# Kernel optimization log

Hardware: AMD Instinct MI355X
Metric: run time of the kernel (lower is better)

Reference implementation:

```python
import jax, jax.numpy as jnp
import numpy as np

B, N, CIN, C = 2, 400000, 192, 128
Y, X, Z = 512, 512, 40
EPS1 = 1e-5   # default BatchNorm1d eps for feature_proj
EPS2 = 1e-3   # norm_fn eps=0.001 for shared_conv BN


def setup_inputs() -> dict:
    key = jax.random.key(0)
    ks = jax.random.split(key, 12)
    voxel_features = jax.random.normal(ks[0], (N, CIN), jnp.float32)
    bi = jax.random.randint(ks[1], (N,), 0, B)
    zi = jax.random.randint(ks[2], (N,), 0, Z)
    yi = jax.random.randint(ks[3], (N,), 0, Y)
    xi = jax.random.randint(ks[4], (N,), 0, X)
    voxel_coords = jnp.stack([bi, zi, yi, xi], axis=1).astype(jnp.int32)  # (N,4)=[b,z,y,x]
    # feature_proj: Linear(CIN->C) + BN1d (inference stats) + ReLU
    W_proj = jax.random.normal(ks[5], (CIN, C), jnp.float32) * np.float32(1.0 / np.sqrt(CIN))
    b_proj = jnp.zeros((C,), jnp.float32)
    bn1_gamma = jnp.ones((C,), jnp.float32)
    bn1_beta = jnp.zeros((C,), jnp.float32)
    bn1_mean = jax.random.normal(ks[6], (C,), jnp.float32) * np.float32(0.1)
    bn1_var = jax.random.uniform(ks[7], (C,), jnp.float32, 0.5, 1.5)
    # shared_conv: SubMConv2d(C,C,3,pad=1,bias) + BN(eps=1e-3) + ReLU
    conv_w = jax.random.normal(ks[8], (3, 3, C, C), jnp.float32) * np.float32(1.0 / np.sqrt(9 * C))
    conv_b = jnp.zeros((C,), jnp.float32)
    bn2_gamma = jnp.ones((C,), jnp.float32)
    bn2_beta = jnp.zeros((C,), jnp.float32)
    bn2_mean = jax.random.normal(ks[9], (C,), jnp.float32) * np.float32(0.1)
    bn2_var = jax.random.uniform(ks[10], (C,), jnp.float32, 0.5, 1.5)
    return dict(voxel_features=voxel_features, voxel_coords=voxel_coords,
                W_proj=W_proj, b_proj=b_proj,
                bn1_gamma=bn1_gamma, bn1_beta=bn1_beta, bn1_mean=bn1_mean, bn1_var=bn1_var,
                conv_w=conv_w, conv_b=conv_b,
                bn2_gamma=bn2_gamma, bn2_beta=bn2_beta, bn2_mean=bn2_mean, bn2_var=bn2_var)


def reference(voxel_features, voxel_coords, W_proj, b_proj,
              bn1_gamma, bn1_beta, bn1_mean, bn1_var,
              conv_w, conv_b, bn2_gamma, bn2_beta, bn2_mean, bn2_var):
    # 1) feature_proj (Linear + BN1d inference + ReLU)
    f = voxel_features @ W_proj + b_proj                      # (N, C)
    f = (f - bn1_mean) * jax.lax.rsqrt(bn1_var + EPS1) * bn1_gamma + bn1_beta
    f = jax.nn.relu(f)
    # 2) bev_aggregate: unique([b,y,x]) + index_add == scatter-sum to dense BEV grid
    bi, yi, xi = voxel_coords[:, 0], voxel_coords[:, 2], voxel_coords[:, 3]
    dense = jnp.zeros((B, Y, X, C), f.dtype).at[bi, yi, xi].add(f)
    active = jnp.zeros((B, Y, X), bool).at[bi, yi, xi].set(True)
    # 3) SubMConv2d(3x3, pad=1) + BN + ReLU; subm == dense conv masked to active sites
    out = jax.lax.conv_general_dilated(dense, conv_w, (1, 1), 'SAME',
                                       dimension_numbers=('NHWC', 'HWIO', 'NHWC')) + conv_b
    out = (out - bn2_mean) * jax.lax.rsqrt(bn2_var + EPS2) * bn2_gamma + bn2_beta
    out = jax.nn.relu(out)
    # sparse tensor only holds active sites; zero elsewhere
    return jnp.where(active[..., None], out, jnp.float32(0.0))  # (B, Y, X, C)
```

## Files before the change

### kernel.cpp

```cpp
#include <hip/hip_runtime.h>

#define Bq 2
#define Yq 512
#define Xq 512
#define NVOX 400000

typedef __bf16 bf16x8 __attribute__((ext_vector_type(8)));
typedef float f32x4 __attribute__((ext_vector_type(4)));
typedef float f32x16 __attribute__((ext_vector_type(16)));
typedef short s16x8 __attribute__((ext_vector_type(8)));
typedef short s16x2 __attribute__((ext_vector_type(2)));

__device__ __forceinline__ short f2bf_s(float f){
    return __builtin_bit_cast(short, static_cast<__bf16>(f));
}

__device__ __forceinline__ void atomic_pk_add_bf16(short* addr, unsigned data){
#if __has_builtin(__builtin_amdgcn_global_atomic_fadd_v2bf16)
    s16x2 v; v[0] = (short)(data & 0xffff); v[1] = (short)(data >> 16);
    __builtin_amdgcn_global_atomic_fadd_v2bf16(
        (__attribute__((address_space(1))) s16x2*)addr, v);
#else
    asm volatile("global_atomic_pk_add_bf16 %0, %1, off"
                 :: "v"(addr), "v"(data) : "memory");
#endif
}

__global__ void kprep(const float* __restrict__ conv_w, const float* __restrict__ W_proj,
                      short* __restrict__ wTs, short* __restrict__ wpT){
    int tid = blockIdx.x*256 + threadIdx.x;
    if (tid < 9*128*128){
        int tap = tid >> 14; int r = tid & 16383; int co = r >> 7; int ci = r & 127;
        int g = ci >> 3, e = ci & 7;
        wTs[tap*16384 + co*128 + (((g & 8) | ((g & 7) ^ (co & 7))) << 3) + e] =
            f2bf_s(conv_w[tap*16384 + ci*128 + co]);
    }
    int e = tid - 9*128*128;
    if (e >= 0 && e < 128*192){
        int co = e / 192; int ci = e - co*192;
        wpT[e] = f2bf_s(W_proj[ci*128 + co]);
    }
}

__global__ void kcount(const int* __restrict__ vc, unsigned* __restrict__ cnt,
                       unsigned char* __restrict__ act){
    int i = blockIdx.x*256 + threadIdx.x;
    if (i >= NVOX) return;
    const int4 c = *reinterpret_cast<const int4*>(vc + i*4);
    int cell = (c.x*Yq + c.z)*Xq + c.w;
    act[cell] = 1;
    atomicAdd(&cnt[cell], 1u);
}

__global__ void __launch_bounds__(256, 2)
kproj(const float* __restrict__ vf, const int* __restrict__ vc,
      const unsigned* __restrict__ cnt,
      const short* __restrict__ wpT, const float* __restrict__ bp,
      const float* __restrict__ g1, const float* __restrict__ be1,
      const float* __restrict__ mu1, const float* __restrict__ va1,
      short* __restrict__ dbf){
    __shared__ char smem[64*200*2];
    __shared__ int cellsPk[64];
    short*    A  = (short*)smem;
    unsigned* st = (unsigned*)smem;
    const int t = threadIdx.x;
    const int v0 = blockIdx.x * 64;

    const float4* vf4 = reinterpret_cast<const float4*>(vf);
    #pragma unroll
    for (int j = 0; j < 12; ++j){
        int i = t + j*256;
        int v = i / 48, kq = i - v*48;
        float4 x = vf4[(size_t)(v0 + v)*48 + kq];
        short4 s; s.x=f2bf_s(x.x); s.y=f2bf_s(x.y); s.z=f2bf_s(x.z); s.w=f2bf_s(x.w);
        *reinterpret_cast<short4*>(&A[v*200 + kq*4]) = s;
    }
    if (t < 64){
        int vi = v0 + t;
        int bi = vc[vi*4 + 0], yi = vc[vi*4 + 2], xi = vc[vi*4 + 3];
        unsigned cn = cnt[(bi*Yq + yi)*Xq + xi];
        int P = (bi*514 + (yi + 1))*514 + (xi + 1);
        cellsPk[t] = (P*8 + ((xi + 1) & 7)) | ((cn > 1) ? (1 << 30) : 0);
    }
    __syncthreads();

    const int w  = t >> 6;
    const int l  = t & 63;
    const int lr = l & 15;
    const int q  = l >> 4;

    const short* wp_lane = wpT + (size_t)(w*32 + lr)*192 + q*8;
    bf16x8 bb[2][6];
    #pragma unroll
    for (int n = 0; n < 2; ++n)
        #pragma unroll
        for (int kc = 0; kc < 6; ++kc)
            bb[n][kc] = *reinterpret_cast<const bf16x8*>(wp_lane + n*16*192 + kc*32);

    f32x4 acc[4][2] = {};
    #pragma unroll
    for (int kc = 0; kc < 6; ++kc){
        bf16x8 a[4];
        #pragma unroll
        for (int m = 0; m < 4; ++m)
            a[m] = *reinterpret_cast<const bf16x8*>(&A[(m*16 + lr)*200 + kc*32 + q*8]);
        #pragma unroll
        for (int m = 0; m < 4; ++m)
            #pragma unroll
            for (int n = 0; n < 2; ++n)
                acc[m][n] = __builtin_amdgcn_mfma_f32_16x16x32_bf16(a[m], bb[n][kc], acc[m][n], 0, 0, 0);
    }

    __syncthreads();
    const int odd = lr & 1;
    #pragma unroll
    for (int n = 0; n < 2; ++n){
        int c = w*32 + n*16 + lr;
        float s1  = g1[c] * rsqrtf(va1[c] + 1e-5f);
        float sh1 = be1[c] + (bp[c] - mu1[c]) * s1;
        int jj = w*16 + n*8 + (lr >> 1);
        #pragma unroll
        for (int m = 0; m < 4; ++m){
            #pragma unroll
            for (int r = 0; r < 4; ++r){
                int vx = m*16 + q*4 + r;
                float val = fmaxf(fmaf(acc[m][n][r], s1, sh1), 0.f);
                float vp  = __shfl_xor(val, 1);
                if (!odd){
                    unsigned data = (unsigned)(unsigned short)f2bf_s(val)
                                  | ((unsigned)(unsigned short)f2bf_s(vp) << 16);
                    st[vx*68 + jj] = data;
                }
            }
        }
    }
    __syncthreads();

    unsigned* dbf_u32 = reinterpret_cast<unsigned*>(dbf);
    #pragma unroll
    for (int i = 0; i < 16; ++i){
        int vv = w*16 + i;
        int pk = cellsPk[vv];
        int multi = pk >> 30;
        int P = (pk & 0x3fffffff) >> 3, xp7 = pk & 7;
        unsigned data = st[vv*68 + l];
        size_t idx = (size_t)P*64 + (((l >> 2) ^ xp7) << 2) + (l & 3);
        if (multi){
            if (data) atomic_pk_add_bf16((short*)(dbf_u32 + idx), data);
        } else {
            dbf_u32[idx] = data;
        }
    }
}

__global__ void __launch_bounds__(512, 2)
kconv(const short* __restrict__ dbf, const short* __restrict__ wTs,
      const unsigned char* __restrict__ act, const float* __restrict__ cb,
      const float* __restrict__ g2, const float* __restrict__ be2,
      const float* __restrict__ mu2, const float* __restrict__ va2,
      float* __restrict__ out){
    __shared__ short Atile[5*1056*8];
    __shared__ short Bbuf[4][1024*8];
    const int t = threadIdx.x;
    const int bid = (blockIdx.x & 7)*256 + (blockIdx.x >> 3);
    const int b   = bid >> 10;
    const int rem = bid & 1023;
    const int y0  = (rem >> 3) << 2;
    const int x0  = (rem & 7) << 6;

    const int w   = t >> 6, l = t & 63;
    const int yy  = w >> 1, nn = w & 1;
    const int l31 = l & 31, hi = l >> 5;
    const int wbase16 = w*64*16;

    #define STAGE_B(BUF, H) do {                                              \
        const short* gb = wTs + (size_t)((H) >> 1)*16384 + ((H) & 1)*64;      \
        _Pragma("unroll")                                                     \
        for (int j = 0; j < 2; ++j){                                          \
            int S = j*512 + t;                                                \
            const short* gp = gb + (S >> 3)*128 + (S & 7)*8;                  \
            __builtin_amdgcn_global_load_lds(                                 \
                (const __attribute__((address_space(1))) void*)gp,            \
                (__attribute__((address_space(3))) void*)                    \
                    ((char*)Bbuf[BUF] + (size_t)(j*512*16) + wbase16), 16, 0, 0); \
        }                                                                     \
    } while(0)

    STAGE_B(0, 0);
    STAGE_B(1, 1);
    #pragma unroll
    for (int j = 0; j < 11; ++j){
        int S = j*512 + t;
        if (S < 5280){
            int r = S / 1056, s = S - r*1056;
            const short* gp = dbf + ((size_t)((b*514 + (y0 + r))*514 + x0)*16 + s)*8;
            __builtin_amdgcn_global_load_lds(
                (const __attribute__((address_space(1))) void*)gp,
                (__attribute__((address_space(3))) void*)
                    ((char*)Atile + (size_t)(j*512*16) + wbase16), 16, 0, 0);
        }
    }

    f32x16 acc[2][2] = {};
    const int bReadBase = (nn*64 + l31)*64;
    const int bXor = l31 & 7;

    #pragma unroll
    for (int p = 0; p < 18; ++p){
        if ((p & 1) == 0){
            __builtin_amdgcn_sched_barrier(0);
            asm volatile("s_waitcnt vmcnt(0)" ::: "memory");
            __builtin_amdgcn_s_barrier();
            __builtin_amdgcn_sched_barrier(0);
            if (p + 2 < 18) STAGE_B((p+2) & 3, p+2);
            if (p + 3 < 18) STAGE_B((p+3) & 3, p+3);
            if (p == 6){
                #pragma unroll
                for (int j = 0; j < 3; ++j){
                    int S = j*512 + t;
                    if (S < 1056){
                        const short* gp = dbf + ((size_t)((b*514 + (y0 + 5))*514 + x0)*16 + S)*8;
                        __builtin_amdgcn_global_load_lds(
                            (const __attribute__((address_space(1))) void*)gp,
                            (__attribute__((address_space(3))) void*)
                                ((char*)Atile + (size_t)(j*512 + w*64)*16), 16, 0, 0);
                    }
                }
            }
            __builtin_amdgcn_sched_barrier(0);
        }
        const short* Bc = Bbuf[p & 3];
        const int tap = p >> 1, hh = p & 1;
        const int ky = tap / 3, kx = tap - ky*3;
        const int row = yy + ky;
        const int rowp = (row >= 5) ? 0 : row;
        const int p0 = l31 + kx, p1 = p0 + 32;
        const int base0 = (rowp*1056 + p0*16)*8;
        const int base1 = (rowp*1056 + p1*16)*8;
        const int pk7 = p0 & 7;
        #pragma unroll
        for (int kc = 0; kc < 4; ++kc){
            const int ks  = kc*2 + hi;
            const int q   = ((hh*8 + ks) ^ pk7) << 3;
            const int qb  = (ks ^ bXor) << 3;
            bf16x8 a0 = *reinterpret_cast<const bf16x8*>(&Atile[base0 + q]);
            bf16x8 a1 = *reinterpret_cast<const bf16x8*>(&Atile[base1 + q]);
            bf16x8 b0 = *reinterpret_cast<const bf16x8*>(&Bc[bReadBase + qb]);
            bf16x8 b1 = *reinterpret_cast<const bf16x8*>(&Bc[bReadBase + 2048 + qb]);
            acc[0][0] = __builtin_amdgcn_mfma_f32_32x32x16_bf16(a0, b0, acc[0][0], 0, 0, 0);
            acc[0][1] = __builtin_amdgcn_mfma_f32_32x32x16_bf16(a0, b1, acc[0][1], 0, 0, 0);
            acc[1][0] = __builtin_amdgcn_mfma_f32_32x32x16_bf16(a1, b0, acc[1][0], 0, 0, 0);
            acc[1][1] = __builtin_amdgcn_mfma_f32_32x32x16_bf16(a1, b1, acc[1][1], 0, 0, 0);
        }
    }
    #undef STAGE_B

    const int yg = y0 + yy;
    const size_t rowcell = (size_t)(b*Yq + yg)*Xq + x0;
    #pragma unroll
    for (int ni = 0; ni < 2; ++ni){
        int c = nn*64 + ni*32 + l31;
        float s2  = g2[c] * rsqrtf(va2[c] + 1e-3f);
        float sh2 = be2[c] + (cb[c] - mu2[c]) * s2;
        #pragma unroll
        for (int mi = 0; mi < 2; ++mi){
            #pragma unroll
            for (int r = 0; r < 16; ++r){
                int pos = mi*32 + (r & 3) + ((r >> 2) << 3) + hi*4;
                size_t cell = rowcell + pos;
                float v = act[cell] ? fmaxf(fmaf(acc[mi][ni][r], s2, sh2), 0.f) : 0.f;
                out[cell*128 + c] = v;
            }
        }
    }
}

extern "C" void kernel_launch(void* const* d_in, const int* in_sizes, int n_in,
                              void* d_out, int out_size, void* d_ws, size_t ws_size,
                              hipStream_t stream){
    const float* vf  = (const float*)d_in[0];
    const int*   vc  = (const int*)  d_in[1];
    const float* Wp  = (const float*)d_in[2];
    const float* bp  = (const float*)d_in[3];
    const float* g1  = (const float*)d_in[4];
    const float* be1 = (const float*)d_in[5];
    const float* mu1 = (const float*)d_in[6];
    const float* va1 = (const float*)d_in[7];
    const float* cw  = (const float*)d_in[8];
    const float* cb  = (const float*)d_in[9];
    const float* g2  = (const float*)d_in[10];
    const float* be2 = (const float*)d_in[11];
    const float* mu2 = (const float*)d_in[12];
    const float* va2 = (const float*)d_in[13];
    float* out = (float*)d_out;
    char* ws = (char*)d_ws;

    if (ws_size < 138233856ull) return;
    short* dbf = (short*)ws;
    unsigned char* act = (unsigned char*)(ws + 135268352);
    short* wTs = (short*)(ws + 135792640);
    short* wpT = (short*)(ws + 136087552);
    unsigned* cnt = (unsigned*)(ws + 136136704);

    hipMemsetAsync(dbf, 0, 135268352, stream);
    hipMemsetAsync(act, 0, 524288, stream);
    hipMemsetAsync(cnt, 0, 2097152, stream);
    kprep<<<672, 256, 0, stream>>>(cw, Wp, wTs, wpT);
    kcount<<<1563, 256, 0, stream>>>(vc, cnt, act);
    kproj<<<6250, 256, 0, stream>>>(vf, vc, cnt, wpT, bp, g1, be1, mu1, va1, dbf);
    kconv<<<2048, 512, 0, stream>>>(dbf, wTs, act, cb, g2, be2, mu2, va2, out);
}
```

Measured before the change: 358.5 us.

## Restructure subm conv: one row per block, weights held in registers per wave

Reworks the conv kernel so each 256-thread block computes one output row of 64 cells. Each wave owns 32 output channels and keeps its bf16 weight fragments in registers, double-buffered across taps and loaded directly from a reordered weight layout produced in the prep kernel. This removes LDS staging of weights and the per-tap barriers. In exchange, each block reloads three halo rows for a single output row, and every block re-reads the full weight set from cache, which raises input and weight traffic.

```diff
diff --git a/kernel.cpp b/kernel.cpp
--- a/kernel.cpp
+++ b/kernel.cpp
@@ -27,12 +27,13 @@
 }
 
 __global__ void kprep(const float* __restrict__ conv_w, const float* __restrict__ W_proj,
-                      short* __restrict__ wTs, short* __restrict__ wpT){
+                      short* __restrict__ wR, short* __restrict__ wpT){
     int tid = blockIdx.x*256 + threadIdx.x;
     if (tid < 9*128*128){
         int tap = tid >> 14; int r = tid & 16383; int co = r >> 7; int ci = r & 127;
-        int g = ci >> 3, e = ci & 7;
-        wTs[tap*16384 + co*128 + (((g & 8) | ((g & 7) ^ (co & 7))) << 3) + e] =
+        int nn = co >> 5, l31 = co & 31;
+        int kcc = ci >> 4, hi = (ci >> 3) & 1, j = ci & 7;
+        wR[(size_t)tap*16384 + nn*4096 + kcc*512 + (hi*32 + l31)*8 + j] =
             f2bf_s(conv_w[tap*16384 + ci*128 + co]);
     }
     int e = tid - 9*128*128;
@@ -153,124 +154,82 @@
     }
 }
 
-__global__ void __launch_bounds__(512, 2)
-kconv(const short* __restrict__ dbf, const short* __restrict__ wTs,
+__global__ void __launch_bounds__(256, 3)
+kconv(const short* __restrict__ dbf, const short* __restrict__ wR,
       const unsigned char* __restrict__ act, const float* __restrict__ cb,
       const float* __restrict__ g2, const float* __restrict__ be2,
       const float* __restrict__ mu2, const float* __restrict__ va2,
       float* __restrict__ out){
-    __shared__ short Atile[5*1056*8];
-    __shared__ short Bbuf[4][1024*8];
+    __shared__ short Atile[3*1056*8];
     const int t = threadIdx.x;
-    const int bid = (blockIdx.x & 7)*256 + (blockIdx.x >> 3);
-    const int b   = bid >> 10;
-    const int rem = bid & 1023;
-    const int y0  = (rem >> 3) << 2;
+    const int bid = (blockIdx.x & 7)*1024 + (blockIdx.x >> 3);
+    const int b   = bid >> 12;
+    const int rem = bid & 4095;
+    const int y   = rem >> 3;
     const int x0  = (rem & 7) << 6;
 
     const int w   = t >> 6, l = t & 63;
-    const int yy  = w >> 1, nn = w & 1;
     const int l31 = l & 31, hi = l >> 5;
-    const int wbase16 = w*64*16;
-
-    #define STAGE_B(BUF, H) do {                                              \
-        const short* gb = wTs + (size_t)((H) >> 1)*16384 + ((H) & 1)*64;      \
-        _Pragma("unroll")                                                     \
-        for (int j = 0; j < 2; ++j){                                          \
-            int S = j*512 + t;                                                \
-            const short* gp = gb + (S >> 3)*128 + (S & 7)*8;                  \
-            __builtin_amdgcn_global_load_lds(                                 \
-                (const __attribute__((address_space(1))) void*)gp,            \
-                (__attribute__((address_space(3))) void*)                    \
-                    ((char*)Bbuf[BUF] + (size_t)(j*512*16) + wbase16), 16, 0, 0); \
-        }                                                                     \
-    } while(0)
-
-    STAGE_B(0, 0);
-    STAGE_B(1, 1);
-    #pragma unroll
-    for (int j = 0; j < 11; ++j){
-        int S = j*512 + t;
-        if (S < 5280){
+
+    #pragma unroll
+    for (int j = 0; j < 13; ++j){
+        int S = j*256 + t;
+        if (S < 3168){
             int r = S / 1056, s = S - r*1056;
-            const short* gp = dbf + ((size_t)((b*514 + (y0 + r))*514 + x0)*16 + s)*8;
+            const short* gp = dbf + ((size_t)((b*514 + (y + r))*514 + x0)*16 + s)*8;
             __builtin_amdgcn_global_load_lds(
                 (const __attribute__((address_space(1))) void*)gp,
                 (__attribute__((address_space(3))) void*)
-                    ((char*)Atile + (size_t)(j*512*16) + wbase16), 16, 0, 0);
-        }
-    }
-
-    f32x16 acc[2][2] = {};
-    const int bReadBase = (nn*64 + l31)*64;
-    const int bXor = l31 & 7;
-
-    #pragma unroll
-    for (int p = 0; p < 18; ++p){
-        if ((p & 1) == 0){
-            __builtin_amdgcn_sched_barrier(0);
-            asm volatile("s_waitcnt vmcnt(0)" ::: "memory");
-            __builtin_amdgcn_s_barrier();
-            __builtin_amdgcn_sched_barrier(0);
-            if (p + 2 < 18) STAGE_B((p+2) & 3, p+2);
-            if (p + 3 < 18) STAGE_B((p+3) & 3, p+3);
-            if (p == 6){
-                #pragma unroll
-                for (int j = 0; j < 3; ++j){
-                    int S = j*512 + t;
-                    if (S < 1056){
-                        const short* gp = dbf + ((size_t)((b*514 + (y0 + 5))*514 + x0)*16 + S)*8;
-                        __builtin_amdgcn_global_load_lds(
-                            (const __attribute__((address_space(1))) void*)gp,
-                            (__attribute__((address_space(3))) void*)
-                                ((char*)Atile + (size_t)(j*512 + w*64)*16), 16, 0, 0);
-                    }
-                }
-            }
-            __builtin_amdgcn_sched_barrier(0);
-        }
-        const short* Bc = Bbuf[p & 3];
-        const int tap = p >> 1, hh = p & 1;
-        const int ky = tap / 3, kx = tap - ky*3;
-        const int row = yy + ky;
-        const int rowp = (row >= 5) ? 0 : row;
+                    ((char*)Atile + (size_t)(j*256 + w*64)*16), 16, 0, 0);
+        }
+    }
+
+    const short* wRb = wR + (size_t)w*4096 + l*8;
+    bf16x8 Breg[2][8];
+    #pragma unroll
+    for (int kcc = 0; kcc < 8; ++kcc)
+        Breg[0][kcc] = *reinterpret_cast<const bf16x8*>(wRb + kcc*512);
+
+    __syncthreads();
+
+    f32x16 acc[2] = {};
+
+    #pragma unroll
+    for (int tp = 0; tp < 9; ++tp){
+        if (tp < 8){
+            const short* wn = wRb + (size_t)(tp+1)*16384;
+            #pragma unroll
+            for (int kcc = 0; kcc < 8; ++kcc)
+                Breg[(tp+1) & 1][kcc] = *reinterpret_cast<const bf16x8*>(wn + kcc*512);
+        }
+        const int ky = tp / 3, kx = tp - ky*3;
         const int p0 = l31 + kx, p1 = p0 + 32;
-        const int base0 = (rowp*1056 + p0*16)*8;
-        const int base1 = (rowp*1056 + p1*16)*8;
+        const int base0 = (ky*1056 + p0*16)*8;
+        const int base1 = (ky*1056 + p1*16)*8;
         const int pk7 = p0 & 7;
         #pragma unroll
-        for (int kc = 0; kc < 4; ++kc){
-            const int ks  = kc*2 + hi;
-            const int q   = ((hh*8 + ks) ^ pk7) << 3;
-            const int qb  = (ks ^ bXor) << 3;
+        for (int kcc = 0; kcc < 8; ++kcc){
+            const int ks = (kcc & 3)*2 + hi, hh = kcc >> 2;
+            const int q  = ((hh*8 + ks) ^ pk7) << 3;
             bf16x8 a0 = *reinterpret_cast<const bf16x8*>(&Atile[base0 + q]);
             bf16x8 a1 = *reinterpret_cast<const bf16x8*>(&Atile[base1 + q]);
-            bf16x8 b0 = *reinterpret_cast<const bf16x8*>(&Bc[bReadBase + qb]);
-            bf16x8 b1 = *reinterpret_cast<const bf16x8*>(&Bc[bReadBase + 2048 + qb]);
-            acc[0][0] = __builtin_amdgcn_mfma_f32_32x32x16_bf16(a0, b0, acc[0][0], 0, 0, 0);
-            acc[0][1] = __builtin_amdgcn_mfma_f32_32x32x16_bf16(a0, b1, acc[0][1], 0, 0, 0);
-            acc[1][0] = __builtin_amdgcn_mfma_f32_32x32x16_bf16(a1, b0, acc[1][0], 0, 0, 0);
-            acc[1][1] = __builtin_amdgcn_mfma_f32_32x32x16_bf16(a1, b1, acc[1][1], 0, 0, 0);
-        }
-    }
-    #undef STAGE_B
-
-    const int yg = y0 + yy;
-    const size_t rowcell = (size_t)(b*Yq + yg)*Xq + x0;
-    #pragma unroll
-    for (int ni = 0; ni < 2; ++ni){
-        int c = nn*64 + ni*32 + l31;
-        float s2  = g2[c] * rsqrtf(va2[c] + 1e-3f);
-        float sh2 = be2[c] + (cb[c] - mu2[c]) * s2;
-        #pragma unroll
-        for (int mi = 0; mi < 2; ++mi){
-            #pragma unroll
-            for (int r = 0; r < 16; ++r){
-                int pos = mi*32 + (r & 3) + ((r >> 2) << 3) + hi*4;
-                size_t cell = rowcell + pos;
-                float v = act[cell] ? fmaxf(fmaf(acc[mi][ni][r], s2, sh2), 0.f) : 0.f;
-                out[cell*128 + c] = v;
-            }
+            acc[0] = __builtin_amdgcn_mfma_f32_32x32x16_bf16(a0, Breg[tp & 1][kcc], acc[0], 0, 0, 0);
+            acc[1] = __builtin_amdgcn_mfma_f32_32x32x16_bf16(a1, Breg[tp & 1][kcc], acc[1], 0, 0, 0);
+        }
+    }
+
+    const int c = w*32 + l31;
+    const float s2  = g2[c] * rsqrtf(va2[c] + 1e-3f);
+    const float sh2 = be2[c] + (cb[c] - mu2[c]) * s2;
+    const size_t rowcell = (size_t)(b*Yq + y)*Xq + x0;
+    #pragma unroll
+    for (int mi = 0; mi < 2; ++mi){
+        #pragma unroll
+        for (int r = 0; r < 16; ++r){
+            int pos = mi*32 + (r & 3) + ((r >> 2) << 3) + hi*4;
+            size_t cell = rowcell + pos;
+            float v = act[cell] ? fmaxf(fmaf(acc[mi][r], s2, sh2), 0.f) : 0.f;
+            out[cell*128 + c] = v;
         }
     }
 }
@@ -298,15 +257,15 @@
     if (ws_size < 138233856ull) return;
     short* dbf = (short*)ws;
     unsigned char* act = (unsigned char*)(ws + 135268352);
-    short* wTs = (short*)(ws + 135792640);
+    short* wR  = (short*)(ws + 135792640);
     short* wpT = (short*)(ws + 136087552);
     unsigned* cnt = (unsigned*)(ws + 136136704);
 
     hipMemsetAsync(dbf, 0, 135268352, stream);
     hipMemsetAsync(act, 0, 524288, stream);
     hipMemsetAsync(cnt, 0, 2097152, stream);
-    kprep<<<672, 256, 0, stream>>>(cw, Wp, wTs, wpT);
+    kprep<<<672, 256, 0, stream>>>(cw, Wp, wR, wpT);
     kcount<<<1563, 256, 0, stream>>>(vc, cnt, act);
     kproj<<<6250, 256, 0, stream>>>(vf, vc, cnt, wpT, bp, g1, be1, mu1, va1, dbf);
-    kconv<<<2048, 512, 0, stream>>>(dbf, wTs, act, cb, g2, be2, mu2, va2, out);
-}
+    kconv<<<8192, 256, 0, stream>>>(dbf, wR, act, cb, g2, be2, mu2, va2, out);
+}
```

After: 363.2 us. About the same (+1.3%).

## Make conv blocks persistent over 16 rows with rolling A-tile ring buffer

Applied to the files above, without the earlier changes.

Each conv block now covers 16 output rows in four groups of four, keeping a 5-row ring of input rows in LDS. Only the new rows are streamed in while earlier groups compute, so each input row is loaded about once instead of being reloaded by every overlapping 4-row block (about 1.25x halo reads instead of 1.5x). The weights are still re-staged each group. Separately, the weight-prep and count kernels are merged into one launch. With only 512 blocks there is less parallelism across CUs and a longer serial chain per block, and the ring indexing adds more complex synchronisation.

```diff
diff --git a/kernel.cpp b/kernel.cpp
--- a/kernel.cpp
+++ b/kernel.cpp
@@ -26,30 +26,33 @@
 #endif
 }
 
-__global__ void kprep(const float* __restrict__ conv_w, const float* __restrict__ W_proj,
-                      short* __restrict__ wTs, short* __restrict__ wpT){
-    int tid = blockIdx.x*256 + threadIdx.x;
-    if (tid < 9*128*128){
-        int tap = tid >> 14; int r = tid & 16383; int co = r >> 7; int ci = r & 127;
-        int g = ci >> 3, e = ci & 7;
-        wTs[tap*16384 + co*128 + (((g & 8) | ((g & 7) ^ (co & 7))) << 3) + e] =
-            f2bf_s(conv_w[tap*16384 + ci*128 + co]);
-    }
-    int e = tid - 9*128*128;
-    if (e >= 0 && e < 128*192){
-        int co = e / 192; int ci = e - co*192;
-        wpT[e] = f2bf_s(W_proj[ci*128 + co]);
-    }
-}
-
-__global__ void kcount(const int* __restrict__ vc, unsigned* __restrict__ cnt,
-                       unsigned char* __restrict__ act){
-    int i = blockIdx.x*256 + threadIdx.x;
-    if (i >= NVOX) return;
-    const int4 c = *reinterpret_cast<const int4*>(vc + i*4);
-    int cell = (c.x*Yq + c.z)*Xq + c.w;
-    act[cell] = 1;
-    atomicAdd(&cnt[cell], 1u);
+__global__ void kinit(const float* __restrict__ conv_w, const float* __restrict__ W_proj,
+                      short* __restrict__ wTs, short* __restrict__ wpT,
+                      const int* __restrict__ vc, unsigned* __restrict__ cnt,
+                      unsigned char* __restrict__ act){
+    const int bx = blockIdx.x;
+    if (bx < 672){
+        int tid = bx*256 + threadIdx.x;
+        if (tid < 9*128*128){
+            int tap = tid >> 14; int r = tid & 16383; int co = r >> 7; int ci = r & 127;
+            int g = ci >> 3, e = ci & 7;
+            wTs[tap*16384 + co*128 + (((g & 8) | ((g & 7) ^ (co & 7))) << 3) + e] =
+                f2bf_s(conv_w[tap*16384 + ci*128 + co]);
+        }
+        int e = tid - 9*128*128;
+        if (e >= 0 && e < 128*192){
+            int co = e / 192; int ci = e - co*192;
+            wpT[e] = f2bf_s(W_proj[ci*128 + co]);
+        }
+    } else {
+        int i = (bx - 672)*256 + threadIdx.x;
+        if (i < NVOX){
+            const int4 c = *reinterpret_cast<const int4*>(vc + i*4);
+            int cell = (c.x*Yq + c.z)*Xq + c.w;
+            act[cell] = 1;
+            atomicAdd(&cnt[cell], 1u);
+        }
+    }
 }
 
 __global__ void __launch_bounds__(256, 2)
@@ -162,10 +165,10 @@
     __shared__ short Atile[5*1056*8];
     __shared__ short Bbuf[4][1024*8];
     const int t = threadIdx.x;
-    const int bid = (blockIdx.x & 7)*256 + (blockIdx.x >> 3);
-    const int b   = bid >> 10;
-    const int rem = bid & 1023;
-    const int y0  = (rem >> 3) << 2;
+    const int bid = (blockIdx.x & 7)*64 + (blockIdx.x >> 3);
+    const int b   = bid >> 8;
+    const int rem = bid & 255;
+    const int y0  = (rem >> 3) << 4;
     const int x0  = (rem & 7) << 6;
 
     const int w   = t >> 6, l = t & 63;
@@ -186,93 +189,105 @@
         }                                                                     \
     } while(0)
 
+    #define STAGE_A(R) do {                                                   \
+        const int slot_ = (R) % 5;                                            \
+        _Pragma("unroll")                                                     \
+        for (int j = 0; j < 3; ++j){                                          \
+            int S = j*512 + t;                                                \
+            if (S < 1056){                                                    \
+                const short* gp = dbf +                                       \
+                    ((size_t)((b*514 + (y0 + (R)))*514 + x0)*16 + S)*8;       \
+                __builtin_amdgcn_global_load_lds(                             \
+                    (const __attribute__((address_space(1))) void*)gp,        \
+                    (__attribute__((address_space(3))) void*)                \
+                        ((char*)Atile + (size_t)(slot_*1056 + j*512 + w*64)*16), \
+                    16, 0, 0);                                                \
+            }                                                                 \
+        }                                                                     \
+    } while(0)
+
     STAGE_B(0, 0);
     STAGE_B(1, 1);
-    #pragma unroll
-    for (int j = 0; j < 11; ++j){
-        int S = j*512 + t;
-        if (S < 5280){
-            int r = S / 1056, s = S - r*1056;
-            const short* gp = dbf + ((size_t)((b*514 + (y0 + r))*514 + x0)*16 + s)*8;
-            __builtin_amdgcn_global_load_lds(
-                (const __attribute__((address_space(1))) void*)gp,
-                (__attribute__((address_space(3))) void*)
-                    ((char*)Atile + (size_t)(j*512*16) + wbase16), 16, 0, 0);
-        }
-    }
-
-    f32x16 acc[2][2] = {};
+    STAGE_A(0); STAGE_A(1); STAGE_A(2); STAGE_A(3); STAGE_A(4);
+
     const int bReadBase = (nn*64 + l31)*64;
     const int bXor = l31 & 7;
 
-    #pragma unroll
-    for (int p = 0; p < 18; ++p){
-        if ((p & 1) == 0){
+    float s2c[2], sh2c[2];
+    #pragma unroll
+    for (int ni = 0; ni < 2; ++ni){
+        int c = nn*64 + ni*32 + l31;
+        s2c[ni]  = g2[c] * rsqrtf(va2[c] + 1e-3f);
+        sh2c[ni] = be2[c] + (cb[c] - mu2[c]) * s2c[ni];
+    }
+
+    #pragma unroll 1
+    for (int g = 0; g < 4; ++g){
+        f32x16 acc[2][2] = {};
+        if (g >= 1){
             __builtin_amdgcn_sched_barrier(0);
-            asm volatile("s_waitcnt vmcnt(0)" ::: "memory");
             __builtin_amdgcn_s_barrier();
             __builtin_amdgcn_sched_barrier(0);
-            if (p + 2 < 18) STAGE_B((p+2) & 3, p+2);
-            if (p + 3 < 18) STAGE_B((p+3) & 3, p+3);
-            if (p == 6){
+            STAGE_A(4*g + 3);
+        }
+        #pragma unroll
+        for (int p = 0; p < 18; ++p){
+            if ((p & 1) == 0){
+                __builtin_amdgcn_sched_barrier(0);
+                asm volatile("s_waitcnt vmcnt(0)" ::: "memory");
+                __builtin_amdgcn_s_barrier();
+                __builtin_amdgcn_sched_barrier(0);
+                const int P = g*18 + p;
+                if (P + 2 < 72) STAGE_B((2*g + p + 2) & 3, (p + 2) % 18);
+                if (P + 3 < 72) STAGE_B((2*g + p + 3) & 3, (p + 3) % 18);
+                if (p == 0 && g >= 1)           STAGE_A(4*g + 4);
+                if (p == 6)                     STAGE_A(4*g + 5);
+                if (p == 12 && (4*g + 6) <= 17) STAGE_A(4*g + 6);
+                __builtin_amdgcn_sched_barrier(0);
+            }
+            const short* Bc = Bbuf[(2*g + p) & 3];
+            const int tap = p >> 1, hh = p & 1;
+            const int ky = tap / 3, kx = tap - ky*3;
+            const int R  = 4*g + yy + ky;
+            const int rowp = R % 5;
+            const int p0 = l31 + kx, p1 = p0 + 32;
+            const int base0 = (rowp*1056 + p0*16)*8;
+            const int base1 = (rowp*1056 + p1*16)*8;
+            const int pk7 = p0 & 7;
+            #pragma unroll
+            for (int kc = 0; kc < 4; ++kc){
+                const int ks  = kc*2 + hi;
+                const int q   = ((hh*8 + ks) ^ pk7) << 3;
+                const int qb  = (ks ^ bXor) << 3;
+                bf16x8 a0 = *reinterpret_cast<const bf16x8*>(&Atile[base0 + q]);
+                bf16x8 a1 = *reinterpret_cast<const bf16x8*>(&Atile[base1 + q]);
+                bf16x8 b0 = *reinterpret_cast<const bf16x8*>(&Bc[bReadBase + qb]);
+                bf16x8 b1 = *reinterpret_cast<const bf16x8*>(&Bc[bReadBase + 2048 + qb]);
+                acc[0][0] = __builtin_amdgcn_mfma_f32_32x32x16_bf16(a0, b0, acc[0][0], 0, 0, 0);
+                acc[0][1] = __builtin_amdgcn_mfma_f32_32x32x16_bf16(a0, b1, acc[0][1], 0, 0, 0);
+                acc[1][0] = __builtin_amdgcn_mfma_f32_32x32x16_bf16(a1, b0, acc[1][0], 0, 0, 0);
+                acc[1][1] = __builtin_amdgcn_mfma_f32_32x32x16_bf16(a1, b1, acc[1][1], 0, 0, 0);
+            }
+        }
+        const int yg = y0 + 4*g + yy;
+        const size_t rowcell = (size_t)(b*Yq + yg)*Xq + x0;
+        #pragma unroll
+        for (int ni = 0; ni < 2; ++ni){
+            int c = nn*64 + ni*32 + l31;
+            #pragma unroll
+            for (int mi = 0; mi < 2; ++mi){
                 #pragma unroll
-                for (int j = 0; j < 3; ++j){
-                    int S = j*512 + t;
-                    if (S < 1056){
-                        const short* gp = dbf + ((size_t)((b*514 + (y0 + 5))*514 + x0)*16 + S)*8;
-                        __builtin_amdgcn_global_load_lds(
-                            (const __attribute__((address_space(1))) void*)gp,
-                            (__attribute__((address_space(3))) void*)
-                                ((char*)Atile + (size_t)(j*512 + w*64)*16), 16, 0, 0);
-                    }
+                for (int r = 0; r < 16; ++r){
+                    int pos = mi*32 + (r & 3) + ((r >> 2) << 3) + hi*4;
+                    size_t cell = rowcell + pos;
+                    float v = act[cell] ? fmaxf(fmaf(acc[mi][ni][r], s2c[ni], sh2c[ni]), 0.f) : 0.f;
+                    out[cell*128 + c] = v;
                 }
             }
-            __builtin_amdgcn_sched_barrier(0);
-        }
-        const short* Bc = Bbuf[p & 3];
-        const int tap = p >> 1, hh = p & 1;
-        const int ky = tap / 3, kx = tap - ky*3;
-        const int row = yy + ky;
-        const int rowp = (row >= 5) ? 0 : row;
-        const int p0 = l31 + kx, p1 = p0 + 32;
-        const int base0 = (rowp*1056 + p0*16)*8;
-        const int base1 = (rowp*1056 + p1*16)*8;
-        const int pk7 = p0 & 7;
-        #pragma unroll
-        for (int kc = 0; kc < 4; ++kc){
-            const int ks  = kc*2 + hi;
-            const int q   = ((hh*8 + ks) ^ pk7) << 3;
-            const int qb  = (ks ^ bXor) << 3;
-            bf16x8 a0 = *reinterpret_cast<const bf16x8*>(&Atile[base0 + q]);
-            bf16x8 a1 = *reinterpret_cast<const bf16x8*>(&Atile[base1 + q]);
-            bf16x8 b0 = *reinterpret_cast<const bf16x8*>(&Bc[bReadBase + qb]);
-            bf16x8 b1 = *reinterpret_cast<const bf16x8*>(&Bc[bReadBase + 2048 + qb]);
-            acc[0][0] = __builtin_amdgcn_mfma_f32_32x32x16_bf16(a0, b0, acc[0][0], 0, 0, 0);
-            acc[0][1] = __builtin_amdgcn_mfma_f32_32x32x16_bf16(a0, b1, acc[0][1], 0, 0, 0);
-            acc[1][0] = __builtin_amdgcn_mfma_f32_32x32x16_bf16(a1, b0, acc[1][0], 0, 0, 0);
-            acc[1][1] = __builtin_amdgcn_mfma_f32_32x32x16_bf16(a1, b1, acc[1][1], 0, 0, 0);
-        }
-    }
+        }
+    }
+    #undef STAGE_A
     #undef STAGE_B
-
-    const int yg = y0 + yy;
-    const size_t rowcell = (size_t)(b*Yq + yg)*Xq + x0;
-    #pragma unroll
-    for (int ni = 0; ni < 2; ++ni){
-        int c = nn*64 + ni*32 + l31;
-        float s2  = g2[c] * rsqrtf(va2[c] + 1e-3f);
-        float sh2 = be2[c] + (cb[c] - mu2[c]) * s2;
-        #pragma unroll
-        for (int mi = 0; mi < 2; ++mi){
-            #pragma unroll
-            for (int r = 0; r < 16; ++r){
-                int pos = mi*32 + (r & 3) + ((r >> 2) << 3) + hi*4;
-                size_t cell = rowcell + pos;
-                float v = act[cell] ? fmaxf(fmaf(acc[mi][ni][r], s2, sh2), 0.f) : 0.f;
-                out[cell*128 + c] = v;
-            }
-        }
-    }
 }
 
 extern "C" void kernel_launch(void* const* d_in, const int* in_sizes, int n_in,
@@ -305,8 +320,7 @@
     hipMemsetAsync(dbf, 0, 135268352, stream);
     hipMemsetAsync(act, 0, 524288, stream);
     hipMemsetAsync(cnt, 0, 2097152, stream);
-    kprep<<<672, 256, 0, stream>>>(cw, Wp, wTs, wpT);
-    kcount<<<1563, 256, 0, stream>>>(vc, cnt, act);
+    kinit<<<2235, 256, 0, stream>>>(cw, Wp, wTs, wpT, vc, cnt, act);
     kproj<<<6250, 256, 0, stream>>>(vf, vc, cnt, wpT, bp, g1, be1, mu1, va1, dbf);
-    kconv<<<2048, 512, 0, stream>>>(dbf, wTs, act, cb, g2, be2, mu2, va2, out);
-}
+    kconv<<<512, 512, 0, stream>>>(dbf, wTs, act, cb, g2, be2, mu2, va2, out);
+}
```

Measured after the change: 354.2 us. About the same (-1.2%).
